# Kernel optimization log

Hardware: AMD Instinct MI355X
Metric: run time of the kernel (lower is better)

Reference implementation:

```python
import jax, jax.numpy as jnp
import numpy as np

PATCH = 3
PAD = PATCH // 2  # stride = 1


def _extract_patches(x):
    """torch F.unfold(k=3, s=1, p=1) reshaped to [b, n=h*w, c*3*3] (c slowest, then ki, kj)."""
    b, c, h, w = x.shape
    xp = jnp.pad(x, ((0, 0), (0, 0), (PAD, PAD), (PAD, PAD)))
    # stack the 9 shifted views -> [b, c, 9, h, w]
    pats = jnp.stack([xp[:, :, i:i + h, j:j + w]
                      for i in range(PATCH) for j in range(PATCH)], axis=2)
    pats = pats.reshape(b, c, PATCH, PATCH, h, w)
    # -> [b, h*w, c*PATCH*PATCH], matching torch unfold channel ordering
    return pats.transpose(0, 4, 5, 1, 2, 3).reshape(b, h * w, c * PATCH * PATCH)


def _l2_normalize(x):
    # F.normalize(dim=2): x / max(||x||_2, 1e-12)
    n = jnp.linalg.norm(x, axis=2, keepdims=True)
    return x / jnp.maximum(n, 1e-12)


def _fold(patches_flat, c, h, w):
    """torch F.fold(k=3, s=1, p=1): overlap-add patches back to [b, c, h, w]."""
    b = patches_flat.shape[0]
    p = patches_flat.reshape(b, h, w, c, PATCH, PATCH)
    out = jnp.zeros((b, c, h + 2 * PAD, w + 2 * PAD), patches_flat.dtype)
    for i in range(PATCH):
        for j in range(PATCH):
            out = out.at[:, :, i:i + h, j:j + w].add(
                p[:, :, :, :, i, j].transpose(0, 3, 1, 2))
    return out[:, :, PAD:PAD + h, PAD:PAD + w]


def setup_inputs() -> dict:
    key = jax.random.key(0)
    k1, k2 = jax.random.split(key)
    B, C, H, W = 1, 256, 96, 96
    return {
        "content_features": jax.random.normal(k1, (B, C, H, W), dtype=jnp.float32),
        "style_features": jax.random.normal(k2, (B, C, H, W), dtype=jnp.float32),
    }


def reference(content_features, style_features):
    b, c, h, w = content_features.shape
    cpat = _extract_patches(content_features)   # [b, n, d]
    spat = _extract_patches(style_features)     # [b, m, d]
    # all-pairs cosine similarity: [b, n, m]
    sim = jnp.einsum('bnd,bmd->bnm', _l2_normalize(cpat), _l2_normalize(spat))
    best = jnp.argmax(sim, axis=2)              # [b, n]
    matched = jnp.take_along_axis(spat, best[:, :, None], axis=1)  # [b, n, d]
    num = _fold(matched, c, h, w)
    den = _fold(jnp.ones_like(matched), c, h, w)
    return num / (den + 1e-8)
```

## Files before the change

### kernel.cpp

```cpp
#include <hip/hip_runtime.h>

#define HH 96
#define WW 96
#define CCH 256
#define NPIX (HH*WW)
#define HP 98
#define NROWS 9604
#define CORE_LO 99
#define CORE_HI 9505

typedef unsigned short u16;
typedef short bf16x8 __attribute__((ext_vector_type(8)));
typedef float f32x4 __attribute__((ext_vector_type(4)));
typedef int i32x4 __attribute__((ext_vector_type(4)));

__device__ __forceinline__ f32x4 ld4u(const float* p) {
    f32x4 r; __builtin_memcpy(&r, p, 16); return r;
}
__device__ __forceinline__ i32x4 ld4ui(const int* p) {
    i32x4 r; __builtin_memcpy(&r, p, 16); return r;
}

__device__ __forceinline__ u16 f2bf_rne(float x) {
    unsigned u = __float_as_uint(x);
    return (u16)((u + 0x7FFFu + ((u >> 16) & 1u)) >> 16);
}

__global__ __launch_bounds__(256) void tobf16_kernel(const float* __restrict__ X,
                                                     u16* __restrict__ HiT,
                                                     u16* __restrict__ LoT) {
    __shared__ u16 hi[64][65], lo[64][65];
    const int n0 = blockIdx.x * 64, k0 = blockIdx.y * 64;
    const int t = threadIdx.x;
    {
        const int kr = t >> 6, nl = t & 63;
#pragma unroll
        for (int r = 0; r < 16; ++r) {
            int kl = kr * 16 + r;
            float x = X[(k0 + kl) * NPIX + n0 + nl];
            u16 h = f2bf_rne(x);
            float hf = __uint_as_float((unsigned)h << 16);
            hi[kl][nl] = h;
            lo[kl][nl] = f2bf_rne(x - hf);
        }
    }
    __syncthreads();
    {
        const int nr = t >> 6, kl = t & 63;
#pragma unroll
        for (int r = 0; r < 16; ++r) {
            int nl = nr * 16 + r;
            HiT[(n0 + nl) * CCH + k0 + kl] = hi[kl][nl];
            LoT[(n0 + nl) * CCH + k0 + kl] = lo[kl][nl];
        }
    }
}

__global__ __launch_bounds__(256) void prep_kernel(const float* __restrict__ Xs,
                                                   float* __restrict__ ssum,
                                                   unsigned long long* __restrict__ keys) {
    int p = blockIdx.x * 256 + threadIdx.x;
    if (p >= NPIX) return;
    float s = 0.f;
#pragma unroll 8
    for (int c = 0; c < CCH; ++c) {
        float v = Xs[c * NPIX + p];
        s = fmaf(v, v, s);
    }
    ssum[p] = s;
    keys[p] = 0ULL;
}

__global__ __launch_bounds__(256) void rnsbp_kernel(const float* __restrict__ ssum,
                                                    float* __restrict__ rnsp,
                                                    float* __restrict__ biasp,
                                                    int* __restrict__ midxp) {
    int mp = blockIdx.x * 256 + threadIdx.x;
    if (mp >= 9632) return;
    int yq = mp / HP, xq = mp - yq * HP;
    bool real = (yq >= 1 && yq <= 96 && xq >= 1 && xq <= 96);
    if (!real) { rnsp[mp] = 0.f; biasp[mp] = -3e38f; midxp[mp] = 0; return; }
    int y = yq - 1, x = xq - 1;
    float s = 0.f;
    for (int dy = -1; dy <= 1; ++dy) {
        int yy = y + dy;
        if ((unsigned)yy >= HH) continue;
        for (int dx = -1; dx <= 1; ++dx) {
            int xx = x + dx;
            if ((unsigned)xx >= WW) continue;
            s += ssum[yy * WW + xx];
        }
    }
    rnsp[mp] = 1.f / fmaxf(sqrtf(s), 1e-12f);
    biasp[mp] = 0.f;
    midxp[mp] = y * WW + x;
}

__global__ __launch_bounds__(256) void padzero_kernel(float* __restrict__ cc, int wstride) {
    int p = blockIdx.x;
    int yq = p / HP, xq = p - yq * HP;
    if (yq >= 1 && yq <= 96 && xq >= 1 && xq <= 96) return;
    const f32x4 z = {0.f, 0.f, 0.f, 0.f};
    float* row = cc + (long long)p * wstride;
    for (int c = threadIdx.x * 4; c < wstride; c += 1024)
        *(f32x4*)&row[c] = z;
}

__global__ __launch_bounds__(256, 2) void cc_gemm_kernel(
        const u16* __restrict__ ChiT, const u16* __restrict__ CloT,
        const u16* __restrict__ ShiT, const u16* __restrict__ SloT,
        float* __restrict__ cc, int csp, int wstride) {
    __shared__ u16 lds[2][4][8][64][8];

    const int tid = threadIdx.x;
    const int n0 = blockIdx.x * 128;
    const int m0 = blockIdx.y * 128;
    const int st = tid >> 5;
    const int la = tid & 31;
    const int arow = n0 + st * 16 + (la & 15);
    const int qp = csp + m0 + st * 16 + (la & 15);
    const int yq = qp / HP, xq = qp - yq * HP;
    const bool okb = (qp < NROWS) && (yq >= 1 && yq <= 96 && xq >= 1 && xq <= 96);
    const int bm = okb ? ((yq - 1) * WW + (xq - 1)) : 0;
    const int kwa = (la >> 4) * 8;

    const u16* pA0 = ChiT + arow * CCH + kwa;
    const u16* pA1 = CloT + arow * CCH + kwa;
    const u16* pB0 = ShiT + bm * CCH + kwa;
    const u16* pB1 = SloT + bm * CCH + kwa;
    const bf16x8 zero = {0, 0, 0, 0, 0, 0, 0, 0};

#define STAGE(buf, kb)                                                          \
    do {                                                                        \
        *(bf16x8*)&lds[buf][0][st][la][0]      = *(const bf16x8*)(pA0 + (kb));  \
        *(bf16x8*)&lds[buf][0][st][la + 32][0] = *(const bf16x8*)(pA0 + (kb) + 16); \
        *(bf16x8*)&lds[buf][1][st][la][0]      = *(const bf16x8*)(pA1 + (kb));  \
        *(bf16x8*)&lds[buf][1][st][la + 32][0] = *(const bf16x8*)(pA1 + (kb) + 16); \
        if (okb) {                                                              \
            *(bf16x8*)&lds[buf][2][st][la][0]      = *(const bf16x8*)(pB0 + (kb));  \
            *(bf16x8*)&lds[buf][2][st][la + 32][0] = *(const bf16x8*)(pB0 + (kb) + 16); \
            *(bf16x8*)&lds[buf][3][st][la][0]      = *(const bf16x8*)(pB1 + (kb));  \
            *(bf16x8*)&lds[buf][3][st][la + 32][0] = *(const bf16x8*)(pB1 + (kb) + 16); \
        } else {                                                                \
            *(bf16x8*)&lds[buf][2][st][la][0] = zero;                           \
            *(bf16x8*)&lds[buf][2][st][la + 32][0] = zero;                      \
            *(bf16x8*)&lds[buf][3][st][la][0] = zero;                           \
            *(bf16x8*)&lds[buf][3][st][la + 32][0] = zero;                      \
        }                                                                       \
    } while (0)

    const int wave = tid >> 6, lane = tid & 63;
    const int wr = wave >> 1, wc = wave & 1;

    f32x4 acc[4][4];
#pragma unroll
    for (int i = 0; i < 4; ++i)
#pragma unroll
        for (int j = 0; j < 4; ++j) acc[i][j] = (f32x4){0.f, 0.f, 0.f, 0.f};

    STAGE(0, 0);
    __syncthreads();

    for (int kk = 0; kk < 8; ++kk) {
        const int cur = kk & 1;
        if (kk < 7) STAGE(cur ^ 1, (kk + 1) * 32);

        bf16x8 ah[4], al[4], bh[4], bl[4];
#pragma unroll
        for (int i = 0; i < 4; ++i) {
            ah[i] = *(const bf16x8*)&lds[cur][0][wr * 4 + i][lane][0];
            al[i] = *(const bf16x8*)&lds[cur][1][wr * 4 + i][lane][0];
            bh[i] = *(const bf16x8*)&lds[cur][2][wc * 4 + i][lane][0];
            bl[i] = *(const bf16x8*)&lds[cur][3][wc * 4 + i][lane][0];
        }
#pragma unroll
        for (int i = 0; i < 4; ++i)
#pragma unroll
            for (int j = 0; j < 4; ++j) {
                acc[i][j] = __builtin_amdgcn_mfma_f32_16x16x32_bf16(ah[i], bh[j], acc[i][j], 0, 0, 0);
                acc[i][j] = __builtin_amdgcn_mfma_f32_16x16x32_bf16(ah[i], bl[j], acc[i][j], 0, 0, 0);
                acc[i][j] = __builtin_amdgcn_mfma_f32_16x16x32_bf16(al[i], bh[j], acc[i][j], 0, 0, 0);
            }
        __syncthreads();
    }
#undef STAGE

    const int r0 = (lane >> 4) * 4;
    const int cl = lane & 15;
#pragma unroll
    for (int i = 0; i < 4; ++i) {
        const int prow = n0 + wr * 64 + i * 16 + r0;
#pragma unroll
        for (int r = 0; r < 4; ++r) {
            const int row = prow + r;
            const int pp = row + 2 * (row / WW) + CORE_LO;
            const long long base = (long long)pp * wstride + m0 + wc * 64 + cl;
#pragma unroll
            for (int j = 0; j < 4; ++j)
                cc[base + j * 16] = acc[i][j][r];
        }
    }
}

__global__ __launch_bounds__(256) void boxsum_kernel(
        const float* __restrict__ cc, const float* __restrict__ rnsp,
        const float* __restrict__ biasp, const int* __restrict__ midxp,
        unsigned long long* __restrict__ keys,
        int core0, int coreEnd, int csp, int wstride) {
    const int wave = threadIdx.x >> 6, lane = threadIdx.x & 63;
    const int n = blockIdx.x * 4 + wave;
    const int pp = n + 2 * (n / WW) + CORE_LO;
    const long long rowbase = (long long)pp * wstride - csp;
    const int W1 = wstride + 1;

    const int OFF[9] = {-99, -98, -97, -1, 0, 1, 97, 98, 99};
    const float* tp[9];
#pragma unroll
    for (int t = 0; t < 9; ++t)
        tp[t] = cc + rowbase + core0 + lane * 4 + (long long)OFF[t] * W1;

    float best = -1e30f;
    int bidx = 0;
    for (int mq = core0 + lane * 4; mq < coreEnd; mq += 256) {
        f32x4 s = {0.f, 0.f, 0.f, 0.f};
#pragma unroll
        for (int t = 0; t < 9; ++t) { s += ld4u(tp[t]); tp[t] += 256; }
        f32x4 rv = ld4u(rnsp + mq);
        f32x4 bv = ld4u(biasp + mq);
        i32x4 iv = ld4ui(midxp + mq);
#pragma unroll
        for (int sl = 0; sl < 4; ++sl) {
            float v = fmaf(s[sl], rv[sl], bv[sl]);
            if (mq + sl >= coreEnd) v = -3e38f;
            if (v > best) { best = v; bidx = iv[sl]; }
        }
    }
#pragma unroll
    for (int d = 32; d; d >>= 1) {
        float ov = __shfl_xor(best, d);
        int oi = __shfl_xor(bidx, d);
        if (ov > best || (ov == best && oi < bidx)) { best = ov; bidx = oi; }
    }
    if (lane == 0) {
        unsigned u = __float_as_uint(best);
        unsigned key = (u & 0x80000000u) ? ~u : (u | 0x80000000u);
        unsigned long long k64 = ((unsigned long long)key << 32)
                               | (unsigned long long)(0xFFFFFFFFu - (unsigned)bidx);
        atomicMax(&keys[n], k64);
    }
}

__global__ __launch_bounds__(256) void fold_kernel(const float* __restrict__ Xs,
                                                   const unsigned long long* __restrict__ keys,
                                                   float* __restrict__ out) {
    int e = blockIdx.x * 256 + threadIdx.x;
    if (e >= CCH * NPIX) return;
    int c = e / NPIX;
    int p = e - c * NPIX;
    int y = p / WW, x = p - y * WW;
    float num = 0.f;
    int den = 0;
#pragma unroll
    for (int i = 0; i < 3; ++i) {
        int ny = y + 1 - i;
        if ((unsigned)ny >= HH) continue;
#pragma unroll
        for (int j = 0; j < 3; ++j) {
            int nx = x + 1 - j;
            if ((unsigned)nx >= WW) continue;
            den++;
            unsigned long long k64 = keys[ny * WW + nx];
            int mg = (int)(0xFFFFFFFFu - (unsigned)(k64 & 0xFFFFFFFFu));
            int my = mg / WW, mx = mg - my * WW;
            int sy = my + i - 1, sx = mx + j - 1;
            if ((unsigned)sy < HH && (unsigned)sx < WW)
                num += Xs[c * NPIX + sy * WW + sx];
        }
    }
    out[e] = num / ((float)den + 1e-8f);
}

extern "C" void kernel_launch(void* const* d_in, const int* in_sizes, int n_in,
                              void* d_out, int out_size, void* d_ws, size_t ws_size,
                              hipStream_t stream) {
    (void)in_sizes; (void)n_in; (void)out_size;
    const float* Xc = (const float*)d_in[0];
    const float* Xs = (const float*)d_in[1];
    float* out = (float*)d_out;

    char* w = (char*)d_ws;
    unsigned long long* keys = (unsigned long long*)w;  w += (size_t)NPIX * 8;
    float* ssum  = (float*)w;                           w += (size_t)NPIX * 4;
    float* rnsp  = (float*)w;                           w += (size_t)9632 * 4;
    float* biasp = (float*)w;                           w += (size_t)9632 * 4;
    int*   midxp = (int*)w;                             w += (size_t)9632 * 4;
    u16* ChiT = (u16*)w;                                w += (size_t)NPIX * CCH * 2;
    u16* CloT = (u16*)w;                                w += (size_t)NPIX * CCH * 2;
    u16* ShiT = (u16*)w;                                w += (size_t)NPIX * CCH * 2;
    u16* SloT = (u16*)w;                                w += (size_t)NPIX * CCH * 2;
    float* ccbuf = (float*)w;
    const size_t fixed = (size_t)(w - (char*)d_ws);

    long long avail = (ws_size > fixed + 4096)
                        ? (long long)(ws_size - fixed - 4096) : 0;
    int wstride = (int)(((avail / ((long long)NROWS * 4)) / 128) * 128);
    if (wstride > 2560) wstride = 2560;
    if (wstride < 512) wstride = 512;
    const int McCore = wstride - 198;

    dim3 gt(NPIX / 64, CCH / 64);
    tobf16_kernel<<<gt, 256, 0, stream>>>(Xc, ChiT, CloT);
    tobf16_kernel<<<gt, 256, 0, stream>>>(Xs, ShiT, SloT);
    prep_kernel<<<NPIX / 256, 256, 0, stream>>>(Xs, ssum, keys);
    rnsbp_kernel<<<38, 256, 0, stream>>>(ssum, rnsp, biasp, midxp);
    padzero_kernel<<<NROWS, 256, 0, stream>>>(ccbuf, wstride);

    for (int core0 = CORE_LO; core0 < CORE_HI; core0 += McCore) {
        int coreEnd = (core0 + McCore < CORE_HI) ? core0 + McCore : CORE_HI;
        int csp = core0 - 99;
        int ce = coreEnd + 99; if (ce > NROWS) ce = NROWS;
        int Wc = ce - csp;
        dim3 g(NPIX / 128, (Wc + 127) / 128);
        cc_gemm_kernel<<<g, 256, 0, stream>>>(ChiT, CloT, ShiT, SloT, ccbuf, csp, wstride);
        boxsum_kernel<<<NPIX / 4, 256, 0, stream>>>(ccbuf, rnsp, biasp, midxp, keys,
                                                    core0, coreEnd, csp, wstride);
    }

    fold_kernel<<<(CCH * NPIX) / 256, 256, 0, stream>>>(Xs, keys, out);
}
```

Measured before the change: 503.6 us.

## Stage GEMM tiles with direct global-to-LDS loads and transpose fold gather

The cc GEMM now uses buffer/global_load_lds to move A and B tiles straight into shared memory, one wave per operand slab. Invalid B rows point at a zeroed scratch buffer instead of branching to write zeros. The fold step now gathers from a channel-last copy of the style features using vector loads, then transposes the result back. This adds two transpose kernels and extra workspace traffic in exchange for coalesced gathers and cheaper GEMM staging.

```diff
diff --git a/kernel.cpp b/kernel.cpp
--- a/kernel.cpp
+++ b/kernel.cpp
@@ -26,6 +26,15 @@
     return (u16)((u + 0x7FFFu + ((u >> 16) & 1u)) >> 16);
 }
 
+__device__ __forceinline__ void stage8(const u16* const* srcs, u16* dst, int kb) {
+#pragma unroll
+    for (int t = 0; t < 8; ++t)
+        __builtin_amdgcn_global_load_lds(
+            (const __attribute__((address_space(1))) unsigned int*)(srcs[t] + kb),
+            (__attribute__((address_space(3))) unsigned int*)(dst + t * 512),
+            16, 0, 0);
+}
+
 __global__ __launch_bounds__(256) void tobf16_kernel(const float* __restrict__ X,
                                                      u16* __restrict__ HiT,
                                                      u16* __restrict__ LoT) {
@@ -54,6 +63,21 @@
             LoT[(n0 + nl) * CCH + k0 + kl] = lo[kl][nl];
         }
     }
+}
+
+__global__ __launch_bounds__(256) void xst_kernel(const float* __restrict__ X,
+                                                  float* __restrict__ XT) {
+    __shared__ float tile[64][65];
+    const int p0 = blockIdx.x * 64, c0 = blockIdx.y * 64;
+    const int t = threadIdx.x;
+    const int rr = t >> 6, cl = t & 63;
+#pragma unroll
+    for (int r = 0; r < 16; ++r)
+        tile[rr * 16 + r][cl] = X[(c0 + rr * 16 + r) * NPIX + p0 + cl];
+    __syncthreads();
+#pragma unroll
+    for (int r = 0; r < 16; ++r)
+        XT[(p0 + rr * 16 + r) * CCH + c0 + cl] = tile[cl][rr * 16 + r];
 }
 
 __global__ __launch_bounds__(256) void prep_kernel(const float* __restrict__ Xs,
@@ -109,48 +133,36 @@
 __global__ __launch_bounds__(256, 2) void cc_gemm_kernel(
         const u16* __restrict__ ChiT, const u16* __restrict__ CloT,
         const u16* __restrict__ ShiT, const u16* __restrict__ SloT,
+        const u16* __restrict__ zbuf,
         float* __restrict__ cc, int csp, int wstride) {
     __shared__ u16 lds[2][4][8][64][8];
 
     const int tid = threadIdx.x;
     const int n0 = blockIdx.x * 128;
     const int m0 = blockIdx.y * 128;
-    const int st = tid >> 5;
-    const int la = tid & 31;
-    const int arow = n0 + st * 16 + (la & 15);
-    const int qp = csp + m0 + st * 16 + (la & 15);
-    const int yq = qp / HP, xq = qp - yq * HP;
-    const bool okb = (qp < NROWS) && (yq >= 1 && yq <= 96 && xq >= 1 && xq <= 96);
-    const int bm = okb ? ((yq - 1) * WW + (xq - 1)) : 0;
-    const int kwa = (la >> 4) * 8;
-
-    const u16* pA0 = ChiT + arow * CCH + kwa;
-    const u16* pA1 = CloT + arow * CCH + kwa;
-    const u16* pB0 = ShiT + bm * CCH + kwa;
-    const u16* pB1 = SloT + bm * CCH + kwa;
-    const bf16x8 zero = {0, 0, 0, 0, 0, 0, 0, 0};
-
-#define STAGE(buf, kb)                                                          \
-    do {                                                                        \
-        *(bf16x8*)&lds[buf][0][st][la][0]      = *(const bf16x8*)(pA0 + (kb));  \
-        *(bf16x8*)&lds[buf][0][st][la + 32][0] = *(const bf16x8*)(pA0 + (kb) + 16); \
-        *(bf16x8*)&lds[buf][1][st][la][0]      = *(const bf16x8*)(pA1 + (kb));  \
-        *(bf16x8*)&lds[buf][1][st][la + 32][0] = *(const bf16x8*)(pA1 + (kb) + 16); \
-        if (okb) {                                                              \
-            *(bf16x8*)&lds[buf][2][st][la][0]      = *(const bf16x8*)(pB0 + (kb));  \
-            *(bf16x8*)&lds[buf][2][st][la + 32][0] = *(const bf16x8*)(pB0 + (kb) + 16); \
-            *(bf16x8*)&lds[buf][3][st][la][0]      = *(const bf16x8*)(pB1 + (kb));  \
-            *(bf16x8*)&lds[buf][3][st][la + 32][0] = *(const bf16x8*)(pB1 + (kb) + 16); \
-        } else {                                                                \
-            *(bf16x8*)&lds[buf][2][st][la][0] = zero;                           \
-            *(bf16x8*)&lds[buf][2][st][la + 32][0] = zero;                      \
-            *(bf16x8*)&lds[buf][3][st][la][0] = zero;                           \
-            *(bf16x8*)&lds[buf][3][st][la + 32][0] = zero;                      \
-        }                                                                       \
-    } while (0)
-
     const int wave = tid >> 6, lane = tid & 63;
     const int wr = wave >> 1, wc = wave & 1;
+    const int rlo = lane & 15, kseg = (lane >> 4) * 8;
+
+    const u16* srcs[8];
+    if (wave < 2) {
+        const u16* base = (wave == 0) ? ChiT : CloT;
+#pragma unroll
+        for (int t = 0; t < 8; ++t)
+            srcs[t] = base + (n0 + t * 16 + rlo) * CCH + kseg;
+    } else {
+        const u16* base = (wave == 2) ? ShiT : SloT;
+#pragma unroll
+        for (int t = 0; t < 8; ++t) {
+            int qp = csp + m0 + t * 16 + rlo;
+            int yq = qp / HP, xq = qp - yq * HP;
+            bool ok = (qp < NROWS) && (yq >= 1 && yq <= 96 && xq >= 1 && xq <= 96);
+            srcs[t] = ok ? (base + ((yq - 1) * WW + (xq - 1)) * CCH + kseg)
+                         : (zbuf + kseg);
+        }
+    }
+    u16* slab0 = &lds[0][wave][0][0][0];
+    u16* slab1 = &lds[1][wave][0][0][0];
 
     f32x4 acc[4][4];
 #pragma unroll
@@ -158,12 +170,12 @@
 #pragma unroll
         for (int j = 0; j < 4; ++j) acc[i][j] = (f32x4){0.f, 0.f, 0.f, 0.f};
 
-    STAGE(0, 0);
+    stage8(srcs, slab0, 0);
     __syncthreads();
 
     for (int kk = 0; kk < 8; ++kk) {
         const int cur = kk & 1;
-        if (kk < 7) STAGE(cur ^ 1, (kk + 1) * 32);
+        if (kk < 7) stage8(srcs, cur ? slab0 : slab1, (kk + 1) * 32);
 
         bf16x8 ah[4], al[4], bh[4], bl[4];
 #pragma unroll
@@ -183,7 +195,6 @@
             }
         __syncthreads();
     }
-#undef STAGE
 
     const int r0 = (lane >> 4) * 4;
     const int cl = lane & 15;
@@ -250,15 +261,13 @@
     }
 }
 
-__global__ __launch_bounds__(256) void fold_kernel(const float* __restrict__ Xs,
-                                                   const unsigned long long* __restrict__ keys,
-                                                   float* __restrict__ out) {
-    int e = blockIdx.x * 256 + threadIdx.x;
-    if (e >= CCH * NPIX) return;
-    int c = e / NPIX;
-    int p = e - c * NPIX;
-    int y = p / WW, x = p - y * WW;
-    float num = 0.f;
+__global__ __launch_bounds__(256) void fold2_kernel(const float* __restrict__ XsT,
+                                                    const unsigned long long* __restrict__ keys,
+                                                    float* __restrict__ outT) {
+    const int wave = threadIdx.x >> 6, lane = threadIdx.x & 63;
+    const int p = blockIdx.x * 4 + wave;
+    const int y = p / WW, x = p - y * WW;
+    f32x4 num = {0.f, 0.f, 0.f, 0.f};
     int den = 0;
 #pragma unroll
     for (int i = 0; i < 3; ++i) {
@@ -274,10 +283,27 @@
             int my = mg / WW, mx = mg - my * WW;
             int sy = my + i - 1, sx = mx + j - 1;
             if ((unsigned)sy < HH && (unsigned)sx < WW)
-                num += Xs[c * NPIX + sy * WW + sx];
-        }
-    }
-    out[e] = num / ((float)den + 1e-8f);
+                num += ld4u(XsT + (long long)(sy * WW + sx) * CCH + lane * 4);
+        }
+    }
+    float inv = 1.f / ((float)den + 1e-8f);
+    f32x4 o = {num[0] * inv, num[1] * inv, num[2] * inv, num[3] * inv};
+    *(f32x4*)&outT[(long long)p * CCH + lane * 4] = o;
+}
+
+__global__ __launch_bounds__(256) void outtr_kernel(const float* __restrict__ outT,
+                                                    float* __restrict__ out) {
+    __shared__ float tile[64][65];
+    const int p0 = blockIdx.x * 64, c0 = blockIdx.y * 64;
+    const int t = threadIdx.x;
+    const int rr = t >> 6, cl = t & 63;
+#pragma unroll
+    for (int r = 0; r < 16; ++r)
+        tile[rr * 16 + r][cl] = outT[(long long)(p0 + rr * 16 + r) * CCH + c0 + cl];
+    __syncthreads();
+#pragma unroll
+    for (int r = 0; r < 16; ++r)
+        out[(long long)(c0 + rr * 16 + r) * NPIX + p0 + cl] = tile[cl][rr * 16 + r];
 }
 
 extern "C" void kernel_launch(void* const* d_in, const int* in_sizes, int n_in,
@@ -294,6 +320,9 @@
     float* rnsp  = (float*)w;                           w += (size_t)9632 * 4;
     float* biasp = (float*)w;                           w += (size_t)9632 * 4;
     int*   midxp = (int*)w;                             w += (size_t)9632 * 4;
+    u16*   zbuf  = (u16*)w;                             w += 1024;
+    float* XsT   = (float*)w;                           w += (size_t)NPIX * CCH * 4;
+    float* outT  = (float*)w;                           w += (size_t)NPIX * CCH * 4;
     u16* ChiT = (u16*)w;                                w += (size_t)NPIX * CCH * 2;
     u16* CloT = (u16*)w;                                w += (size_t)NPIX * CCH * 2;
     u16* ShiT = (u16*)w;                                w += (size_t)NPIX * CCH * 2;
@@ -308,9 +337,11 @@
     if (wstride < 512) wstride = 512;
     const int McCore = wstride - 198;
 
+    hipMemsetAsync(zbuf, 0, 1024, stream);
     dim3 gt(NPIX / 64, CCH / 64);
     tobf16_kernel<<<gt, 256, 0, stream>>>(Xc, ChiT, CloT);
     tobf16_kernel<<<gt, 256, 0, stream>>>(Xs, ShiT, SloT);
+    xst_kernel<<<gt, 256, 0, stream>>>(Xs, XsT);
     prep_kernel<<<NPIX / 256, 256, 0, stream>>>(Xs, ssum, keys);
     rnsbp_kernel<<<38, 256, 0, stream>>>(ssum, rnsp, biasp, midxp);
     padzero_kernel<<<NROWS, 256, 0, stream>>>(ccbuf, wstride);
@@ -321,10 +352,12 @@
         int ce = coreEnd + 99; if (ce > NROWS) ce = NROWS;
         int Wc = ce - csp;
         dim3 g(NPIX / 128, (Wc + 127) / 128);
-        cc_gemm_kernel<<<g, 256, 0, stream>>>(ChiT, CloT, ShiT, SloT, ccbuf, csp, wstride);
+        cc_gemm_kernel<<<g, 256, 0, stream>>>(ChiT, CloT, ShiT, SloT, zbuf,
+                                              ccbuf, csp, wstride);
         boxsum_kernel<<<NPIX / 4, 256, 0, stream>>>(ccbuf, rnsp, biasp, midxp, keys,
                                                     core0, coreEnd, csp, wstride);
     }
 
-    fold_kernel<<<(CCH * NPIX) / 256, 256, 0, stream>>>(Xs, keys, out);
-}
+    fold2_kernel<<<NPIX / 4, 256, 0, stream>>>(XsT, keys, outT);
+    outtr_kernel<<<gt, 256, 0, stream>>>(outT, out);
+}
```

Result: faster. 452.5 us (-10.1%).
